# Kernel tuning notes

Hardware: AMD Instinct MI355X
Metric: run time of the kernel (lower is better)

## Reference

```python
import jax, jax.numpy as jnp
import numpy as np

N = 20000          # nodes
DEG = 8            # deterministic in-degree per node
E = N * DEG        # edges
IN_DIM = 16
HID = 128
EDGE_DIM = 8
OUT_DIM = 4
LN_EPS = 1e-5
# degree histogram has all mass at DEG -> avg log-degree = log(DEG + 1)
AVG_DEG_LOG = float(np.log(DEG + 1.0))


def _init(key, fan_in, fan_out):
    s = float(np.sqrt(2.0 / (fan_in + fan_out)))  # glorot-ish
    return jax.random.normal(key, (fan_in, fan_out), jnp.float32) * s


def setup_inputs() -> dict:
    key = jax.random.key(0)
    ks = jax.random.split(key, 24)
    x = jax.random.normal(ks[0], (N, IN_DIM), jnp.float32)
    src = jax.random.randint(ks[1], (E,), 0, N, jnp.int32)
    dst = (jnp.arange(E, dtype=jnp.int32) % N)  # every node has exactly DEG in-edges
    edge_index = jnp.stack([src, dst], axis=0)
    edge_attr = jax.random.normal(ks[2], (E, EDGE_DIM), jnp.float32)
    d = {"x": x, "edge_attr": edge_attr, "edge_index": edge_index}
    i = 3
    for l, fi in enumerate([IN_DIM, HID]):  # 2 PNAConv layers (num_layers=3)
        d[f"ew{l}"] = _init(ks[i], EDGE_DIM, fi); i += 1   # edge_encoder
        d[f"eb{l}"] = jnp.zeros((fi,), jnp.float32)
        d[f"pw{l}"] = _init(ks[i], 3 * fi, fi); i += 1     # pre_nn: cat(x_i,x_j,e)
        d[f"pb{l}"] = jnp.zeros((fi,), jnp.float32)
        d[f"qw{l}"] = _init(ks[i], 13 * fi, HID); i += 1   # post_nn: (4 aggr * 3 scalers + 1)*F_in
        d[f"qb{l}"] = jnp.zeros((HID,), jnp.float32)
        d[f"lw{l}"] = _init(ks[i], HID, HID); i += 1       # PNAConv.lin
        d[f"lb{l}"] = jnp.zeros((HID,), jnp.float32)
        d[f"g{l}"] = jnp.ones((HID,), jnp.float32)         # LayerNorm gamma
        d[f"b{l}"] = jnp.zeros((HID,), jnp.float32)        # LayerNorm beta
    d["hw"] = _init(ks[i], HID, OUT_DIM)
    d["hb"] = jnp.zeros((OUT_DIM,), jnp.float32)
    return d


def _pna_conv(x, src, dst, edge_attr, ew, eb, pw, pb, qw, qb, lw, lb):
    # messages: cat(x_i, x_j, edge_encoder(edge_attr)) -> pre MLP
    e = edge_attr @ ew + eb                                   # [E, F_in]
    h = jnp.concatenate([x[dst], x[src], e], axis=-1)         # [E, 3*F_in]
    h = h @ pw + pb                                           # [E, F_in]
    # multi-aggregator reduce by destination node
    deg = jax.ops.segment_sum(jnp.ones((E,), h.dtype), dst, num_segments=N)
    degc = jnp.maximum(deg, 1.0)[:, None]
    mean = jax.ops.segment_sum(h, dst, num_segments=N) / degc
    mean2 = jax.ops.segment_sum(h * h, dst, num_segments=N) / degc
    mx = jax.ops.segment_max(h, dst, num_segments=N)
    mn = jax.ops.segment_min(h, dst, num_segments=N)
    std = jnp.sqrt(jax.nn.relu(mean2 - mean * mean) + 1e-5)
    agg = jnp.concatenate([mean, mx, mn, std], axis=-1)       # [N, 4*F_in]
    # degree scalers: identity, amplification, attenuation (scaler-major layout)
    logd = jnp.log(deg + 1.0)[:, None]
    scaled = jnp.concatenate(
        [agg, agg * (logd / AVG_DEG_LOG), agg * (AVG_DEG_LOG / logd)], axis=-1
    )                                                         # [N, 12*F_in]
    out = jnp.concatenate([x, scaled], axis=-1) @ qw + qb     # post_nn, [N, F_out]
    return out @ lw + lb                                      # PNAConv.lin


def _ln(x, g, b):
    m = jnp.mean(x, axis=-1, keepdims=True)
    v = jnp.mean((x - m) ** 2, axis=-1, keepdims=True)
    return (x - m) / jnp.sqrt(v + LN_EPS) * g + b


def reference(x, edge_attr, ew0, eb0, pw0, pb0, qw0, qb0, lw0, lb0, g0, b0,
              ew1, eb1, pw1, pb1, qw1, qb1, lw1, lb1, g1, b1, hw, hb, edge_index):
    src, dst = edge_index[0], edge_index[1]
    h = _pna_conv(x, src, dst, edge_attr, ew0, eb0, pw0, pb0, qw0, qb0, lw0, lb0)
    h = jax.nn.relu(_ln(h, g0, b0))  # dropout is identity at inference
    h = _pna_conv(h, src, dst, edge_attr, ew1, eb1, pw1, pb1, qw1, qb1, lw1, lb1)
    h = jax.nn.relu(_ln(h, g1, b1))
    return h @ hw + hb               # head, [N, OUT_DIM]
```

## Files before the change

### kernel.cpp

```cpp
#include <hip/hip_runtime.h>
#include <math.h>

#define N_NODES 20000
#define N_EDGES 160000

typedef unsigned short ushort_t;
typedef __attribute__((ext_vector_type(8))) short short8v;
typedef __attribute__((ext_vector_type(4))) float f32x4;
typedef __attribute__((ext_vector_type(8))) float f32x8;

#define WS_We0  0
#define WS_b0m  128
#define WS_W0   256
#define WS_b0   10496
#define WS_We1  10624
#define WS_b1m  11648
#define WS_b1   11776
#define WS_WP1  11904
#define WS_WPTU 52864
#define WS_t0   69248
#define WS_u0   389248
#define WS_h0b  709248
#define WS_t1   1989248
#define WS_u1   4549248
#define WS_A0   7109248
#define WS_A1   7109248

__device__ inline ushort_t f2bf(float f) {
    union { float f; unsigned u; } v; v.f = f;
    unsigned r = v.u + 0x7FFFu + ((v.u >> 16) & 1u);
    return (ushort_t)(r >> 16);
}

__global__ __launch_bounds__(256) void k_prep(
    const float* __restrict__ x,
    const float* __restrict__ ew0, const float* __restrict__ eb0,
    const float* __restrict__ pw0, const float* __restrict__ pb0,
    const float* __restrict__ qw0, const float* __restrict__ qb0,
    const float* __restrict__ lw0, const float* __restrict__ lb0,
    const float* __restrict__ ew1, const float* __restrict__ eb1,
    const float* __restrict__ pw1, const float* __restrict__ pb1,
    const float* __restrict__ qw1, const float* __restrict__ qb1,
    const float* __restrict__ lw1, const float* __restrict__ lb1,
    float* __restrict__ ws)
{
    int tid = blockIdx.x * 256 + threadIdx.x;
    if (tid < 81920) {
        int r = tid >> 7, o = tid & 127;
        float acc = 0.f;
        for (int h = 0; h < 128; ++h) {
            float qr;
            if (r < 128) qr = qw1[r*128 + h];
            else {
                int s = r - 128;
                qr = qw1[(128+s)*128+h] + qw1[(640+s)*128+h] + qw1[(1152+s)*128+h];
            }
            acc += qr * lw1[h*128 + o];
        }
        int ct = o >> 4, ks = r >> 5;
        int l = (o & 15) | (((r >> 3) & 3) << 4);
        ((ushort_t*)(ws + WS_WP1))[(size_t)(((ct*20 + ks)*64) + l)*8 + (r & 7)] = f2bf(acc);
    } else if (tid < 82048) {
        int o = tid - 81920;
        float acc = lb1[o];
        for (int h = 0; h < 128; ++h) acc += qb1[h] * lw1[h*128 + o];
        ws[WS_b1 + o] = acc;
    } else if (tid < 92288) {
        int idx = tid - 82048; int r = idx >> 7, o = idx & 127;
        float acc = 0.f;
        for (int h = 0; h < 128; ++h) {
            float qr;
            if (r < 16) qr = qw0[r*128 + h];
            else {
                int s = r - 16;
                qr = qw0[(16+s)*128+h] + qw0[(80+s)*128+h] + qw0[(144+s)*128+h];
            }
            acc += qr * lw0[h*128 + o];
        }
        ws[WS_W0 + idx] = acc;
    } else if (tid < 92416) {
        int o = tid - 92288;
        float acc = lb0[o];
        for (int h = 0; h < 128; ++h) acc += qb0[h] * lw0[h*128 + o];
        ws[WS_b0 + o] = acc;
    } else if (tid < 93440) {
        int idx = tid - 92416; int c = idx >> 7, f = idx & 127;
        float acc = 0.f;
        for (int k = 0; k < 128; ++k) acc += ew1[c*128 + k] * pw1[(256+k)*128 + f];
        ws[WS_We1 + idx] = acc;
    } else if (tid < 93568) {
        int f = tid - 93440;
        float acc = pb1[f];
        for (int k = 0; k < 128; ++k) acc += eb1[k] * pw1[(256+k)*128 + f];
        ws[WS_b1m + f] = acc;
    } else if (tid < 93696) {
        int idx = tid - 93568; int c = idx >> 4, f = idx & 15;
        float acc = 0.f;
        for (int k = 0; k < 16; ++k) acc += ew0[c*16 + k] * pw0[(32+k)*16 + f];
        ws[WS_We0 + idx] = acc;
    } else if (tid < 93712) {
        int f = tid - 93696;
        float acc = pb0[f];
        for (int k = 0; k < 16; ++k) acc += eb0[k] * pw0[(32+k)*16 + f];
        ws[WS_b0m + f] = acc;
    } else if (tid < 126480) {
        int idx = tid - 93712;
        int r = idx >> 7, o = idx & 127;
        int part = r >> 7, rk = r & 127;
        int ct = part*8 + (o >> 4);
        int l = (o & 15) | (((rk >> 3) & 3) << 4);
        ((ushort_t*)(ws + WS_WPTU))[(size_t)(((ct*4 + (rk >> 5))*64) + l)*8 + (rk & 7)]
            = f2bf(pw1[r*128 + o]);
    } else if (tid < 446480) {
        int idx = tid - 126480; int i = idx >> 4, f = idx & 15;
        float acc = 0.f;
        for (int k = 0; k < 16; ++k) acc += x[i*16 + k] * pw0[k*16 + f];
        ws[WS_t0 + idx] = acc;
    } else if (tid < 766480) {
        int idx = tid - 446480; int i = idx >> 4, f = idx & 15;
        float acc = 0.f;
        for (int k = 0; k < 16; ++k) acc += x[i*16 + k] * pw0[(16+k)*16 + f];
        ws[WS_u0 + idx] = acc;
    }
}

__global__ __launch_bounds__(256) void k_agg0(
    const float* __restrict__ x, const float* __restrict__ ea,
    const int* __restrict__ src, float* __restrict__ ws)
{
    __shared__ float ea_s[16*8*8];
    __shared__ int   src_s[16*8];
    __shared__ float We0_s[128];
    __shared__ float b0m_s[16];
    const int t = threadIdx.x;
    const int i0 = blockIdx.x * 16;

    for (int idx = t; idx < 1024; idx += 256) {
        int k = idx >> 7; int rem = idx & 127; int n = rem >> 3, c = rem & 7;
        ea_s[(n*8 + k)*8 + c] = ea[(i0 + n + k*N_NODES)*8 + c];
    }
    if (t < 128) {
        int k = t >> 4, n = t & 15;
        src_s[n*8 + k] = src[i0 + n + k*N_NODES];
        We0_s[t] = ws[WS_We0 + t];
    }
    if (t < 16) b0m_s[t] = ws[WS_b0m + t];
    __syncthreads();

    const int n = t >> 4, f = t & 15;
    const int i = i0 + n;
    float base = ws[WS_t0 + i*16 + f] + b0m_s[f];
    float s = 0.f, q = 0.f, mx = -1e30f, mn = 1e30f;
    for (int k = 0; k < 8; ++k) {
        int sj = src_s[n*8 + k];
        float m = base + ws[WS_u0 + sj*16 + f];
        #pragma unroll
        for (int c = 0; c < 8; ++c) m += ea_s[(n*8+k)*8 + c] * We0_s[c*16 + f];
        s += m; q += m*m; mx = fmaxf(mx, m); mn = fminf(mn, m);
    }
    float mean = s * 0.125f, mean2 = q * 0.125f;
    float sd = sqrtf(fmaxf(mean2 - mean*mean, 0.f) + 1e-5f);
    float* A0 = ws + WS_A0 + (size_t)i * 80;
    A0[f]      = x[i*16 + f];
    A0[16 + f] = mean;
    A0[32 + f] = mx;
    A0[48 + f] = mn;
    A0[64 + f] = sd;
}

__global__ __launch_bounds__(256) void k_gemm0(
    const float* __restrict__ g0, const float* __restrict__ bln0,
    float* __restrict__ ws)
{
    __shared__ float As[32][81];
    const int t = threadIdx.x;
    const int r0 = blockIdx.x * 32;
    const float* A = ws + WS_A0 + (size_t)r0 * 80;
    for (int idx = t; idx < 32*80; idx += 256) {
        int r = idx / 80, k = idx - r*80;
        As[r][k] = A[idx];
    }
    __syncthreads();
    const int tc = t & 31, tr = t >> 5;
    const int c0 = tc * 4;
    float acc[4][4] = {};
    const float* W = ws + WS_W0;
    #pragma unroll 4
    for (int k = 0; k < 80; ++k) {
        float4 b = *(const float4*)(W + k*128 + c0);
        #pragma unroll
        for (int rr = 0; rr < 4; ++rr) {
            float a = As[tr*4 + rr][k];
            acc[rr][0] += a*b.x; acc[rr][1] += a*b.y;
            acc[rr][2] += a*b.z; acc[rr][3] += a*b.w;
        }
    }
    float4 bias = *(const float4*)(ws + WS_b0 + c0);
    float4 g  = *(const float4*)(g0 + c0);
    float4 bb = *(const float4*)(bln0 + c0);
    ushort_t* h0b = (ushort_t*)(ws + WS_h0b);
    #pragma unroll
    for (int rr = 0; rr < 4; ++rr) {
        float v0 = acc[rr][0] + bias.x, v1 = acc[rr][1] + bias.y;
        float v2 = acc[rr][2] + bias.z, v3 = acc[rr][3] + bias.w;
        float sum = v0+v1+v2+v3;
        float sq  = v0*v0+v1*v1+v2*v2+v3*v3;
        #pragma unroll
        for (int off = 1; off < 32; off <<= 1) {
            sum += __shfl_xor(sum, off, 64);
            sq  += __shfl_xor(sq,  off, 64);
        }
        float mean = sum * (1.f/128.f);
        float var  = sq  * (1.f/128.f) - mean*mean;
        float rstd = rsqrtf(var + 1e-5f);
        ushort4 ob;
        ob.x = f2bf(fmaxf((v0-mean)*rstd*g.x + bb.x, 0.f));
        ob.y = f2bf(fmaxf((v1-mean)*rstd*g.y + bb.y, 0.f));
        ob.z = f2bf(fmaxf((v2-mean)*rstd*g.z + bb.z, 0.f));
        ob.w = f2bf(fmaxf((v3-mean)*rstd*g.w + bb.w, 0.f));
        *(ushort4*)(h0b + (size_t)(r0 + tr*4 + rr)*128 + c0) = ob;
    }
}

__global__ __launch_bounds__(64) void k_tu1(float* __restrict__ ws)
{
    const int lane = threadIdx.x;
    const int rowbase = blockIdx.x * 16;
    const ushort_t* h0b = (const ushort_t*)(ws + WS_h0b);
    const ushort_t* WP  = (const ushort_t*)(ws + WS_WPTU);
    const int lr = lane & 15, lk = lane >> 4;
    const size_t arow = rowbase + lr;
    f32x4 acc[16];
    #pragma unroll
    for (int c = 0; c < 16; ++c) acc[c] = (f32x4){0.f,0.f,0.f,0.f};

    #pragma unroll
    for (int ks = 0; ks < 4; ++ks) {
        short8v a = *(const short8v*)(h0b + arow*128 + ks*32 + lk*8);
        #pragma unroll
        for (int c = 0; c < 16; ++c) {
            short8v b = *(const short8v*)(WP + ((size_t)(c*4 + ks)*64 + lane)*8);
            acc[c] = __builtin_amdgcn_mfma_f32_16x16x32_bf16(a, b, acc[c], 0, 0, 0);
        }
    }
    float* t1 = ws + WS_t1;
    float* u1 = ws + WS_u1;
    #pragma unroll
    for (int c = 0; c < 16; ++c) {
        float* dst = (c < 8) ? t1 : u1;
        int cb = (c & 7)*16 + lr;
        #pragma unroll
        for (int r = 0; r < 4; ++r) {
            int row = rowbase + lk*4 + r;
            dst[(size_t)row*128 + cb] = acc[c][r];
        }
    }
}

__global__ __launch_bounds__(256) void k_agg1(
    const float* __restrict__ ea, const int* __restrict__ src,
    float* __restrict__ ws)
{
    __shared__ float ea_s[16*8*8];
    __shared__ int   src_s[128];
    __shared__ float We1_s[1024];
    __shared__ float b1m_s[128];
    const int t = threadIdx.x;
    const int i0 = blockIdx.x * 16;

    for (int idx = t; idx < 1024; idx += 256) {
        int k = idx >> 7; int rem = idx & 127; int n = rem >> 3, c = rem & 7;
        ea_s[(n*8 + k)*8 + c] = ea[(i0 + n + k*N_NODES)*8 + c];
    }
    if (t < 128) {
        int k = t >> 4, n = t & 15;
        src_s[n*8 + k] = src[i0 + n + k*N_NODES];
    }
    for (int idx = t; idx < 1024; idx += 256) We1_s[idx] = ws[WS_We1 + idx];
    if (t < 128) b1m_s[t] = ws[WS_b1m + t];
    __syncthreads();

    const int n = t >> 4, f0 = (t & 15) * 8;
    const int i = i0 + n;
    float base[8], sm[8], sq[8], mx[8], mn[8];
    #pragma unroll
    for (int e = 0; e < 8; ++e) {
        base[e] = ws[WS_t1 + (size_t)i*128 + f0 + e] + b1m_s[f0 + e];
        sm[e] = 0.f; sq[e] = 0.f; mx[e] = -1e30f; mn[e] = 1e30f;
    }
    for (int k = 0; k < 8; ++k) {
        int sj = src_s[n*8 + k];
        const float* urow = ws + WS_u1 + (size_t)sj*128 + f0;
        float m[8];
        #pragma unroll
        for (int e = 0; e < 8; ++e) m[e] = base[e] + urow[e];
        #pragma unroll
        for (int c = 0; c < 8; ++c) {
            float a = ea_s[(n*8 + k)*8 + c];
            #pragma unroll
            for (int e = 0; e < 8; ++e) m[e] += a * We1_s[c*128 + f0 + e];
        }
        #pragma unroll
        for (int e = 0; e < 8; ++e) {
            sm[e] += m[e]; sq[e] += m[e]*m[e];
            mx[e] = fmaxf(mx[e], m[e]); mn[e] = fminf(mn[e], m[e]);
        }
    }
    ushort_t* A1 = (ushort_t*)(ws + WS_A1);
    short8v vm, vx, vn, vs;
    #pragma unroll
    for (int e = 0; e < 8; ++e) {
        float mean = sm[e]*0.125f, m2 = sq[e]*0.125f;
        float sd = sqrtf(fmaxf(m2 - mean*mean, 0.f) + 1e-5f);
        vm[e] = (short)f2bf(mean);
        vx[e] = (short)f2bf(mx[e]);
        vn[e] = (short)f2bf(mn[e]);
        vs[e] = (short)f2bf(sd);
    }
    size_t b = (size_t)i*512 + f0;
    *(short8v*)(A1 + b)       = vm;
    *(short8v*)(A1 + b + 128) = vx;
    *(short8v*)(A1 + b + 256) = vn;
    *(short8v*)(A1 + b + 384) = vs;
}

__global__ __launch_bounds__(128) void k_gemm1(
    const float* __restrict__ g1, const float* __restrict__ bln1,
    const float* __restrict__ hw, const float* __restrict__ hb,
    float* __restrict__ ws, float* __restrict__ out)
{
    __shared__ float redS[2][16], redQ[2][16];
    __shared__ f32x4 redP[16];
    const int t = threadIdx.x;
    const int w = t >> 6, lane = t & 63;
    const int lr = lane & 15, lk = lane >> 4;
    const int rowbase = blockIdx.x * 16;
    const int row = rowbase + lr;
    const ushort_t* h0b = (const ushort_t*)(ws + WS_h0b);
    const ushort_t* A1  = (const ushort_t*)(ws + WS_A1);
    const ushort_t* WP  = (const ushort_t*)(ws + WS_WP1);

    f32x4 acc[4];
    #pragma unroll
    for (int c = 0; c < 4; ++c) acc[c] = (f32x4){0.f,0.f,0.f,0.f};

    #pragma unroll
    for (int kw = 0; kw < 4; ++kw) {
        short8v a = *(const short8v*)(h0b + (size_t)row*128 + kw*32 + lk*8);
        #pragma unroll
        for (int c = 0; c < 4; ++c) {
            int ct = w*4 + c;
            short8v b = *(const short8v*)(WP + (size_t)((ct*20 + kw)*64 + lane)*8);
            acc[c] = __builtin_amdgcn_mfma_f32_16x16x32_bf16(a, b, acc[c], 0, 0, 0);
        }
    }
    #pragma unroll 4
    for (int ks = 0; ks < 16; ++ks) {
        short8v a = *(const short8v*)(A1 + (size_t)row*512 + ks*32 + lk*8);
        #pragma unroll
        for (int c = 0; c < 4; ++c) {
            int ct = w*4 + c;
            short8v b = *(const short8v*)(WP + (size_t)((ct*20 + 4 + ks)*64 + lane)*8);
            acc[c] = __builtin_amdgcn_mfma_f32_16x16x32_bf16(a, b, acc[c], 0, 0, 0);
        }
    }

    float bc[4], gc[4], bbc[4]; f32x4 hwc[4];
    #pragma unroll
    for (int c = 0; c < 4; ++c) {
        int col = (w*4 + c)*16 + lr;
        bc[c]  = ws[WS_b1 + col];
        gc[c]  = g1[col];
        bbc[c] = bln1[col];
        hwc[c] = *(const f32x4*)(hw + col*4);
    }

    #pragma unroll
    for (int r = 0; r < 4; ++r) {
        float s = 0.f, q = 0.f;
        #pragma unroll
        for (int c = 0; c < 4; ++c) {
            float v = acc[c][r] + bc[c];
            s += v; q += v*v;
        }
        #pragma unroll
        for (int off = 1; off < 16; off <<= 1) {
            s += __shfl_xor(s, off, 64);
            q += __shfl_xor(q, off, 64);
        }
        if (lr == 0) { redS[w][lk*4 + r] = s; redQ[w][lk*4 + r] = q; }
    }
    __syncthreads();

    f32x4 poarr[4];
    #pragma unroll
    for (int r = 0; r < 4; ++r) {
        int orow = lk*4 + r;
        float s_tot = redS[0][orow] + redS[1][orow];
        float q_tot = redQ[0][orow] + redQ[1][orow];
        float mean = s_tot * (1.f/128.f);
        float var  = q_tot * (1.f/128.f) - mean*mean;
        float rstd = rsqrtf(var + 1e-5f);
        f32x4 po = (f32x4){0.f,0.f,0.f,0.f};
        #pragma unroll
        for (int c = 0; c < 4; ++c) {
            float v = acc[c][r] + bc[c];
            float o = fmaxf((v-mean)*rstd*gc[c] + bbc[c], 0.f);
            po += o * hwc[c];
        }
        #pragma unroll
        for (int off = 1; off < 16; off <<= 1) {
            po.x += __shfl_xor(po.x, off, 64);
            po.y += __shfl_xor(po.y, off, 64);
            po.z += __shfl_xor(po.z, off, 64);
            po.w += __shfl_xor(po.w, off, 64);
        }
        poarr[r] = po;
        if (w == 1 && lr == 0) redP[orow] = po;
    }
    __syncthreads();

    if (w == 0 && lr == 0) {
        f32x4 hb4 = *(const f32x4*)hb;
        #pragma unroll
        for (int r = 0; r < 4; ++r) {
            int orow = lk*4 + r;
            f32x4 res = poarr[r] + redP[orow] + hb4;
            *(f32x4*)(out + (size_t)(rowbase + orow)*4) = res;
        }
    }
}

extern "C" void kernel_launch(void* const* d_in, const int* in_sizes, int n_in,
                              void* d_out, int out_size, void* d_ws, size_t ws_size,
                              hipStream_t stream)
{
    const float* x    = (const float*)d_in[0];
    const float* ea   = (const float*)d_in[1];
    const int*   eidx = (const int*)d_in[2];
    const float* ew0  = (const float*)d_in[3];
    const float* eb0  = (const float*)d_in[4];
    const float* pw0  = (const float*)d_in[5];
    const float* pb0  = (const float*)d_in[6];
    const float* qw0  = (const float*)d_in[7];
    const float* qb0  = (const float*)d_in[8];
    const float* lw0  = (const float*)d_in[9];
    const float* lb0  = (const float*)d_in[10];
    const float* g0   = (const float*)d_in[11];
    const float* bl0  = (const float*)d_in[12];
    const float* ew1  = (const float*)d_in[13];
    const float* eb1  = (const float*)d_in[14];
    const float* pw1  = (const float*)d_in[15];
    const float* pb1  = (const float*)d_in[16];
    const float* qw1  = (const float*)d_in[17];
    const float* qb1  = (const float*)d_in[18];
    const float* lw1  = (const float*)d_in[19];
    const float* lb1  = (const float*)d_in[20];
    const float* g1   = (const float*)d_in[21];
    const float* bl1  = (const float*)d_in[22];
    const float* hw   = (const float*)d_in[23];
    const float* hb   = (const float*)d_in[24];
    const int* src = eidx;
    float* ws = (float*)d_ws;
    float* out = (float*)d_out;

    k_prep<<<2995, 256, 0, stream>>>(x, ew0, eb0, pw0, pb0, qw0, qb0, lw0, lb0,
                                     ew1, eb1, pw1, pb1, qw1, qb1, lw1, lb1, ws);
    k_agg0<<<1250, 256, 0, stream>>>(x, ea, src, ws);
    k_gemm0<<<625, 256, 0, stream>>>(g0, bl0, ws);
    k_tu1<<<1250, 64, 0, stream>>>(ws);
    k_agg1<<<1250, 256, 0, stream>>>(ea, src, ws);
    k_gemm1<<<1250, 128, 0, stream>>>(g1, bl1, hw, hb, ws, out);
}
```

Measured before the change: 112.6 us.

## Fuse agg0/gemm0/tu1 and agg1/gemm1 into two per-tile kernels

Merges the five post-prep kernels into two: k_mid runs layer-0 aggregation, the layer-0 GEMM+LayerNorm and the t1/u1 projection per 32-row tile, and k_tail runs layer-1 aggregation plus the final GEMM and head. Row-local dependencies are satisfied inside a block with barriers, and only the global gather on u1 needs a kernel boundary. This removes three launches and the inter-kernel drains. In exchange it uses fewer, heavier blocks, noinline device calls and more shared memory per block, which may reduce occupancy.

```diff
diff --git a/kernel.cpp b/kernel.cpp
--- a/kernel.cpp
+++ b/kernel.cpp
@@ -32,8 +32,8 @@
     return (ushort_t)(r >> 16);
 }
 
-__global__ __launch_bounds__(256) void k_prep(
-    const float* __restrict__ x,
+__device__ __attribute__((noinline)) void prep_item(
+    int tid, const float* __restrict__ x,
     const float* __restrict__ ew0, const float* __restrict__ eb0,
     const float* __restrict__ pw0, const float* __restrict__ pb0,
     const float* __restrict__ qw0, const float* __restrict__ qb0,
@@ -44,7 +44,6 @@
     const float* __restrict__ lw1, const float* __restrict__ lb1,
     float* __restrict__ ws)
 {
-    int tid = blockIdx.x * 256 + threadIdx.x;
     if (tid < 81920) {
         int r = tid >> 7, o = tid & 127;
         float acc = 0.f;
@@ -124,38 +123,38 @@
     }
 }
 
-__global__ __launch_bounds__(256) void k_agg0(
-    const float* __restrict__ x, const float* __restrict__ ea,
+__device__ __attribute__((noinline)) void agg0_tile(
+    int tile, int t, const float* __restrict__ x, const float* __restrict__ ea,
     const int* __restrict__ src, float* __restrict__ ws)
 {
-    __shared__ float ea_s[16*8*8];
-    __shared__ int   src_s[16*8];
-    __shared__ float We0_s[128];
-    __shared__ float b0m_s[16];
-    const int t = threadIdx.x;
-    const int i0 = blockIdx.x * 16;
+    static __shared__ float ea_s0[16*8*8];
+    static __shared__ int   src_s0[16*8];
+    static __shared__ float We0_s0[128];
+    static __shared__ float b0m_s0[16];
+    const int i0 = tile * 16;
+    __syncthreads();
 
     for (int idx = t; idx < 1024; idx += 256) {
         int k = idx >> 7; int rem = idx & 127; int n = rem >> 3, c = rem & 7;
-        ea_s[(n*8 + k)*8 + c] = ea[(i0 + n + k*N_NODES)*8 + c];
+        ea_s0[(n*8 + k)*8 + c] = ea[(i0 + n + k*N_NODES)*8 + c];
     }
     if (t < 128) {
         int k = t >> 4, n = t & 15;
-        src_s[n*8 + k] = src[i0 + n + k*N_NODES];
-        We0_s[t] = ws[WS_We0 + t];
-    }
-    if (t < 16) b0m_s[t] = ws[WS_b0m + t];
+        src_s0[n*8 + k] = src[i0 + n + k*N_NODES];
+        We0_s0[t] = ws[WS_We0 + t];
+    }
+    if (t < 16) b0m_s0[t] = ws[WS_b0m + t];
     __syncthreads();
 
     const int n = t >> 4, f = t & 15;
     const int i = i0 + n;
-    float base = ws[WS_t0 + i*16 + f] + b0m_s[f];
+    float base = ws[WS_t0 + i*16 + f] + b0m_s0[f];
     float s = 0.f, q = 0.f, mx = -1e30f, mn = 1e30f;
     for (int k = 0; k < 8; ++k) {
-        int sj = src_s[n*8 + k];
+        int sj = src_s0[n*8 + k];
         float m = base + ws[WS_u0 + sj*16 + f];
         #pragma unroll
-        for (int c = 0; c < 8; ++c) m += ea_s[(n*8+k)*8 + c] * We0_s[c*16 + f];
+        for (int c = 0; c < 8; ++c) m += ea_s0[(n*8+k)*8 + c] * We0_s0[c*16 + f];
         s += m; q += m*m; mx = fmaxf(mx, m); mn = fminf(mn, m);
     }
     float mean = s * 0.125f, mean2 = q * 0.125f;
@@ -168,13 +167,13 @@
     A0[64 + f] = sd;
 }
 
-__global__ __launch_bounds__(256) void k_gemm0(
-    const float* __restrict__ g0, const float* __restrict__ bln0,
+__device__ __attribute__((noinline)) void gemm0_tile(
+    int tile, int t, const float* __restrict__ g0, const float* __restrict__ bln0,
     float* __restrict__ ws)
 {
-    __shared__ float As[32][81];
-    const int t = threadIdx.x;
-    const int r0 = blockIdx.x * 32;
+    static __shared__ float As[32][81];
+    const int r0 = tile * 32;
+    __syncthreads();
     const float* A = ws + WS_A0 + (size_t)r0 * 80;
     for (int idx = t; idx < 32*80; idx += 256) {
         int r = idx / 80, k = idx - r*80;
@@ -222,33 +221,31 @@
     }
 }
 
-__global__ __launch_bounds__(64) void k_tu1(float* __restrict__ ws)
-{
-    const int lane = threadIdx.x;
-    const int rowbase = blockIdx.x * 16;
+__device__ __attribute__((noinline)) void tu1_half(
+    int tile, int part, int lane, float* __restrict__ ws)
+{
+    const int rowbase = tile * 16;
     const ushort_t* h0b = (const ushort_t*)(ws + WS_h0b);
     const ushort_t* WP  = (const ushort_t*)(ws + WS_WPTU);
     const int lr = lane & 15, lk = lane >> 4;
     const size_t arow = rowbase + lr;
-    f32x4 acc[16];
-    #pragma unroll
-    for (int c = 0; c < 16; ++c) acc[c] = (f32x4){0.f,0.f,0.f,0.f};
+    f32x4 acc[8];
+    #pragma unroll
+    for (int c = 0; c < 8; ++c) acc[c] = (f32x4){0.f,0.f,0.f,0.f};
 
     #pragma unroll
     for (int ks = 0; ks < 4; ++ks) {
         short8v a = *(const short8v*)(h0b + arow*128 + ks*32 + lk*8);
         #pragma unroll
-        for (int c = 0; c < 16; ++c) {
-            short8v b = *(const short8v*)(WP + ((size_t)(c*4 + ks)*64 + lane)*8);
+        for (int c = 0; c < 8; ++c) {
+            short8v b = *(const short8v*)(WP + ((size_t)((part*8 + c)*4 + ks)*64 + lane)*8);
             acc[c] = __builtin_amdgcn_mfma_f32_16x16x32_bf16(a, b, acc[c], 0, 0, 0);
         }
     }
-    float* t1 = ws + WS_t1;
-    float* u1 = ws + WS_u1;
-    #pragma unroll
-    for (int c = 0; c < 16; ++c) {
-        float* dst = (c < 8) ? t1 : u1;
-        int cb = (c & 7)*16 + lr;
+    float* dst = part ? (ws + WS_u1) : (ws + WS_t1);
+    #pragma unroll
+    for (int c = 0; c < 8; ++c) {
+        int cb = c*16 + lr;
         #pragma unroll
         for (int r = 0; r < 4; ++r) {
             int row = rowbase + lk*4 + r;
@@ -257,27 +254,27 @@
     }
 }
 
-__global__ __launch_bounds__(256) void k_agg1(
-    const float* __restrict__ ea, const int* __restrict__ src,
+__device__ __attribute__((noinline)) void agg1_tile(
+    int tile, int t, const float* __restrict__ ea, const int* __restrict__ src,
     float* __restrict__ ws)
 {
-    __shared__ float ea_s[16*8*8];
-    __shared__ int   src_s[128];
-    __shared__ float We1_s[1024];
-    __shared__ float b1m_s[128];
-    const int t = threadIdx.x;
-    const int i0 = blockIdx.x * 16;
+    static __shared__ float ea_s1[16*8*8];
+    static __shared__ int   src_s1[128];
+    static __shared__ float We1_s1[1024];
+    static __shared__ float b1m_s1[128];
+    const int i0 = tile * 16;
+    __syncthreads();
 
     for (int idx = t; idx < 1024; idx += 256) {
         int k = idx >> 7; int rem = idx & 127; int n = rem >> 3, c = rem & 7;
-        ea_s[(n*8 + k)*8 + c] = ea[(i0 + n + k*N_NODES)*8 + c];
+        ea_s1[(n*8 + k)*8 + c] = ea[(i0 + n + k*N_NODES)*8 + c];
     }
     if (t < 128) {
         int k = t >> 4, n = t & 15;
-        src_s[n*8 + k] = src[i0 + n + k*N_NODES];
-    }
-    for (int idx = t; idx < 1024; idx += 256) We1_s[idx] = ws[WS_We1 + idx];
-    if (t < 128) b1m_s[t] = ws[WS_b1m + t];
+        src_s1[n*8 + k] = src[i0 + n + k*N_NODES];
+    }
+    for (int idx = t; idx < 1024; idx += 256) We1_s1[idx] = ws[WS_We1 + idx];
+    if (t < 128) b1m_s1[t] = ws[WS_b1m + t];
     __syncthreads();
 
     const int n = t >> 4, f0 = (t & 15) * 8;
@@ -285,20 +282,20 @@
     float base[8], sm[8], sq[8], mx[8], mn[8];
     #pragma unroll
     for (int e = 0; e < 8; ++e) {
-        base[e] = ws[WS_t1 + (size_t)i*128 + f0 + e] + b1m_s[f0 + e];
+        base[e] = ws[WS_t1 + (size_t)i*128 + f0 + e] + b1m_s1[f0 + e];
         sm[e] = 0.f; sq[e] = 0.f; mx[e] = -1e30f; mn[e] = 1e30f;
     }
     for (int k = 0; k < 8; ++k) {
-        int sj = src_s[n*8 + k];
+        int sj = src_s1[n*8 + k];
         const float* urow = ws + WS_u1 + (size_t)sj*128 + f0;
         float m[8];
         #pragma unroll
         for (int e = 0; e < 8; ++e) m[e] = base[e] + urow[e];
         #pragma unroll
         for (int c = 0; c < 8; ++c) {
-            float a = ea_s[(n*8 + k)*8 + c];
+            float a = ea_s1[(n*8 + k)*8 + c];
             #pragma unroll
-            for (int e = 0; e < 8; ++e) m[e] += a * We1_s[c*128 + f0 + e];
+            for (int e = 0; e < 8; ++e) m[e] += a * We1_s1[c*128 + f0 + e];
         }
         #pragma unroll
         for (int e = 0; e < 8; ++e) {
@@ -324,17 +321,17 @@
     *(short8v*)(A1 + b + 384) = vs;
 }
 
-__global__ __launch_bounds__(128) void k_gemm1(
+__device__ __attribute__((noinline)) void gemm1_tile(
+    int tile, int tl, int hf,
     const float* __restrict__ g1, const float* __restrict__ bln1,
     const float* __restrict__ hw, const float* __restrict__ hb,
     float* __restrict__ ws, float* __restrict__ out)
 {
-    __shared__ float redS[2][16], redQ[2][16];
-    __shared__ f32x4 redP[16];
-    const int t = threadIdx.x;
-    const int w = t >> 6, lane = t & 63;
+    static __shared__ float redS[2][2][16], redQ[2][2][16];
+    static __shared__ f32x4 redP[2][16];
+    const int w = tl >> 6, lane = tl & 63;
     const int lr = lane & 15, lk = lane >> 4;
-    const int rowbase = blockIdx.x * 16;
+    const int rowbase = tile * 16;
     const int row = rowbase + lr;
     const ushort_t* h0b = (const ushort_t*)(ws + WS_h0b);
     const ushort_t* A1  = (const ushort_t*)(ws + WS_A1);
@@ -388,7 +385,7 @@
             s += __shfl_xor(s, off, 64);
             q += __shfl_xor(q, off, 64);
         }
-        if (lr == 0) { redS[w][lk*4 + r] = s; redQ[w][lk*4 + r] = q; }
+        if (lr == 0) { redS[hf][w][lk*4 + r] = s; redQ[hf][w][lk*4 + r] = q; }
     }
     __syncthreads();
 
@@ -396,8 +393,8 @@
     #pragma unroll
     for (int r = 0; r < 4; ++r) {
         int orow = lk*4 + r;
-        float s_tot = redS[0][orow] + redS[1][orow];
-        float q_tot = redQ[0][orow] + redQ[1][orow];
+        float s_tot = redS[hf][0][orow] + redS[hf][1][orow];
+        float q_tot = redQ[hf][0][orow] + redQ[hf][1][orow];
         float mean = s_tot * (1.f/128.f);
         float var  = q_tot * (1.f/128.f) - mean*mean;
         float rstd = rsqrtf(var + 1e-5f);
@@ -416,7 +413,7 @@
             po.w += __shfl_xor(po.w, off, 64);
         }
         poarr[r] = po;
-        if (w == 1 && lr == 0) redP[orow] = po;
+        if (w == 1 && lr == 0) redP[hf][orow] = po;
     }
     __syncthreads();
 
@@ -425,50 +422,79 @@
         #pragma unroll
         for (int r = 0; r < 4; ++r) {
             int orow = lk*4 + r;
-            f32x4 res = poarr[r] + redP[orow] + hb4;
+            f32x4 res = poarr[r] + redP[hf][orow] + hb4;
             *(f32x4*)(out + (size_t)(rowbase + orow)*4) = res;
         }
     }
+}
+
+struct KArgs {
+    const float *x, *ea; const int* src;
+    const float *ew0,*eb0,*pw0,*pb0,*qw0,*qb0,*lw0,*lb0,*g0,*bl0;
+    const float *ew1,*eb1,*pw1,*pb1,*qw1,*qb1,*lw1,*lb1,*g1,*bl1;
+    const float *hw,*hb;
+    float* ws; float* out;
+};
+
+__global__ __launch_bounds__(256) void k_prep(KArgs a) {
+    int tid = blockIdx.x*256 + threadIdx.x;
+    prep_item(tid, a.x, a.ew0, a.eb0, a.pw0, a.pb0, a.qw0, a.qb0, a.lw0, a.lb0,
+              a.ew1, a.eb1, a.pw1, a.pb1, a.qw1, a.qb1, a.lw1, a.lb1, a.ws);
+}
+
+__global__ __launch_bounds__(256) void k_mid(KArgs a) {
+    const int b = blockIdx.x, t = threadIdx.x;
+    agg0_tile(b*2,     t, a.x, a.ea, a.src, a.ws);
+    agg0_tile(b*2 + 1, t, a.x, a.ea, a.src, a.ws);
+    gemm0_tile(b, t, a.g0, a.bl0, a.ws);
+    __syncthreads();
+    const int w = t >> 6;
+    tu1_half(b*2 + (w >> 1), w & 1, t & 63, a.ws);
+}
+
+__global__ __launch_bounds__(256) void k_tail(KArgs a) {
+    const int b = blockIdx.x, t = threadIdx.x;
+    agg1_tile(b*2,     t, a.ea, a.src, a.ws);
+    agg1_tile(b*2 + 1, t, a.ea, a.src, a.ws);
+    __syncthreads();
+    const int hf = t >> 7;
+    gemm1_tile(b*2 + hf, t & 127, hf, a.g1, a.bl1, a.hw, a.hb, a.ws, a.out);
 }
 
 extern "C" void kernel_launch(void* const* d_in, const int* in_sizes, int n_in,
                               void* d_out, int out_size, void* d_ws, size_t ws_size,
                               hipStream_t stream)
 {
-    const float* x    = (const float*)d_in[0];
-    const float* ea   = (const float*)d_in[1];
-    const int*   eidx = (const int*)d_in[2];
-    const float* ew0  = (const float*)d_in[3];
-    const float* eb0  = (const float*)d_in[4];
-    const float* pw0  = (const float*)d_in[5];
-    const float* pb0  = (const float*)d_in[6];
-    const float* qw0  = (const float*)d_in[7];
-    const float* qb0  = (const float*)d_in[8];
-    const float* lw0  = (const float*)d_in[9];
-    const float* lb0  = (const float*)d_in[10];
-    const float* g0   = (const float*)d_in[11];
-    const float* bl0  = (const float*)d_in[12];
-    const float* ew1  = (const float*)d_in[13];
-    const float* eb1  = (const float*)d_in[14];
-    const float* pw1  = (const float*)d_in[15];
-    const float* pb1  = (const float*)d_in[16];
-    const float* qw1  = (const float*)d_in[17];
-    const float* qb1  = (const float*)d_in[18];
-    const float* lw1  = (const float*)d_in[19];
-    const float* lb1  = (const float*)d_in[20];
-    const float* g1   = (const float*)d_in[21];
-    const float* bl1  = (const float*)d_in[22];
-    const float* hw   = (const float*)d_in[23];
-    const float* hb   = (const float*)d_in[24];
-    const int* src = eidx;
-    float* ws = (float*)d_ws;
-    float* out = (float*)d_out;
-
-    k_prep<<<2995, 256, 0, stream>>>(x, ew0, eb0, pw0, pb0, qw0, qb0, lw0, lb0,
-                                     ew1, eb1, pw1, pb1, qw1, qb1, lw1, lb1, ws);
-    k_agg0<<<1250, 256, 0, stream>>>(x, ea, src, ws);
-    k_gemm0<<<625, 256, 0, stream>>>(g0, bl0, ws);
-    k_tu1<<<1250, 64, 0, stream>>>(ws);
-    k_agg1<<<1250, 256, 0, stream>>>(ea, src, ws);
-    k_gemm1<<<1250, 128, 0, stream>>>(g1, bl1, hw, hb, ws, out);
-}
+    KArgs a;
+    a.x    = (const float*)d_in[0];
+    a.ea   = (const float*)d_in[1];
+    a.src  = (const int*)d_in[2];
+    a.ew0  = (const float*)d_in[3];
+    a.eb0  = (const float*)d_in[4];
+    a.pw0  = (const float*)d_in[5];
+    a.pb0  = (const float*)d_in[6];
+    a.qw0  = (const float*)d_in[7];
+    a.qb0  = (const float*)d_in[8];
+    a.lw0  = (const float*)d_in[9];
+    a.lb0  = (const float*)d_in[10];
+    a.g0   = (const float*)d_in[11];
+    a.bl0  = (const float*)d_in[12];
+    a.ew1  = (const float*)d_in[13];
+    a.eb1  = (const float*)d_in[14];
+    a.pw1  = (const float*)d_in[15];
+    a.pb1  = (const float*)d_in[16];
+    a.qw1  = (const float*)d_in[17];
+    a.qb1  = (const float*)d_in[18];
+    a.lw1  = (const float*)d_in[19];
+    a.lb1  = (const float*)d_in[20];
+    a.g1   = (const float*)d_in[21];
+    a.bl1  = (const float*)d_in[22];
+    a.hw   = (const float*)d_in[23];
+    a.hb   = (const float*)d_in[24];
+    a.ws   = (float*)d_ws;
+    a.out  = (float*)d_out;
+
+    k_prep<<<2995, 256, 0, stream>>>(a);
+    k_mid <<< 625, 256, 0, stream>>>(a);
+    k_tail<<< 625, 256, 0, stream>>>(a);
+}
```

Measured after the change: 117.3 us. +4.2%, slower.
